# Performance work log

Hardware: AMD Instinct MI355X
Metric: run time of the kernel (lower is better)

## Reference

```python
import jax, jax.numpy as jnp
import numpy as np

N_EMBED = 1024
N_HEAD = 16
HEAD_SIZE = N_EMBED // N_HEAD  # 64
SEQ = 2048
BATCH = 2
EPS = 1e-5


def setup_inputs() -> dict:
    key = jax.random.key(0)
    ks = jax.random.split(key, 16)
    s = lambda fan_in: 1.0 / np.sqrt(fan_in)
    d, h, hs, f = N_EMBED, N_HEAD, HEAD_SIZE, 4 * N_EMBED
    return {
        "x": jax.random.normal(ks[0], (BATCH, SEQ, d), dtype=jnp.float32),
        # per-head QKV projections (no bias), stacked over heads: [H, D, hs]
        "wq": jax.random.normal(ks[1], (h, d, hs), dtype=jnp.float32) * s(d),
        "wk": jax.random.normal(ks[2], (h, d, hs), dtype=jnp.float32) * s(d),
        "wv": jax.random.normal(ks[3], (h, d, hs), dtype=jnp.float32) * s(d),
        "w_proj": jax.random.normal(ks[4], (d, d), dtype=jnp.float32) * s(d),
        "b_proj": jnp.zeros((d,), dtype=jnp.float32),
        "w1": jax.random.normal(ks[5], (d, f), dtype=jnp.float32) * s(d),
        "b1": jnp.zeros((f,), dtype=jnp.float32),
        "w2": jax.random.normal(ks[6], (f, d), dtype=jnp.float32) * s(f),
        "b2": jnp.zeros((d,), dtype=jnp.float32),
        "g1": jnp.ones((d,), dtype=jnp.float32),
        "be1": jnp.zeros((d,), dtype=jnp.float32),
        "g2": jnp.ones((d,), dtype=jnp.float32),
        "be2": jnp.zeros((d,), dtype=jnp.float32),
    }


def _layer_norm(x, gamma, beta):
    mu = jnp.mean(x, axis=-1, keepdims=True)
    var = jnp.mean(jnp.square(x - mu), axis=-1, keepdims=True)
    return (x - mu) * jax.lax.rsqrt(var + EPS) * gamma + beta


def reference(x, wq, wk, wv, w_proj, b_proj, w1, b1, w2, b2, g1, be1, g2, be2):
    B, S, D = x.shape
    # per-head projections (vectorized over heads): [B, H, S, hs]
    q = jnp.einsum("bsd,hdk->bhsk", x, wq)
    k = jnp.einsum("bsd,hdk->bhsk", x, wk)
    v = jnp.einsum("bsd,hdk->bhsk", x, wv)
    scale = HEAD_SIZE ** -0.5
    scores = jnp.einsum("bhsk,bhtk->bhst", q, k) * scale  # [B,H,S,S]
    causal = jnp.tril(jnp.ones((S, S), dtype=bool))
    scores = jnp.where(causal, scores, -jnp.inf)
    w = jax.nn.softmax(scores, axis=-1)  # dropout=0 -> identity
    attn = jnp.einsum("bhst,bhtk->bhsk", w, v)  # [B,H,S,hs]
    # concat heads (head-major ordering matches torch.cat over heads)
    attn = attn.transpose(0, 2, 1, 3).reshape(B, S, D)
    y = attn @ w_proj + b_proj
    x = _layer_norm(x + y, g1, be1)
    y = jax.nn.relu(x @ w1 + b1) @ w2 + b2
    x = _layer_norm(x + y, g2, be2)
    return x
```

## Files before the change

kernel.cpp:

```cpp
#include <hip/hip_runtime.h>


typedef unsigned short u16;
typedef unsigned int u32;
typedef __attribute__((ext_vector_type(8))) short bf16x8;
typedef __attribute__((ext_vector_type(4))) float f32x4;
typedef __attribute__((ext_vector_type(2))) u32 u32x2;
typedef __attribute__((ext_vector_type(4))) _Float16 f16x4;

#define MFMA16(a, b, c) __builtin_amdgcn_mfma_f32_16x16x32_bf16(a, b, c, 0, 0, 0)
#define MFMAH(a, b, c) __builtin_amdgcn_mfma_f32_16x16x16f16(a, b, c, 0, 0, 0)

__device__ __forceinline__ u16 f2b(float f) {
  unsigned int u = __builtin_bit_cast(unsigned int, f);
  u = (u + 0x7fffu + ((u >> 16) & 1u)) >> 16;
  return (u16)u;
}

__device__ __forceinline__ void gload_lds16(const u16* g, u16* l) {
  __builtin_amdgcn_global_load_lds((const __attribute__((address_space(1))) void*)g,
                                   (__attribute__((address_space(3))) void*)l, 16, 0, 0);
}

__device__ __forceinline__ u32 pkrtz(float lo, float hi) {
  return __builtin_bit_cast(u32, __builtin_amdgcn_cvt_pkrtz(lo, hi));
}

__device__ __forceinline__ f16x4 pack4h(float a, float b, float c, float d) {
  u32x2 r = {pkrtz(a, b), pkrtz(c, d)};
  return __builtin_bit_cast(f16x4, r);
}

__device__ __forceinline__ u16 f2h(float v) {
  return __builtin_bit_cast(u16, (_Float16)v);
}


__global__ __launch_bounds__(256) void castx_kernel(const float* __restrict__ src,
                                                    u16* __restrict__ dst) {
  int i = (blockIdx.x * 256 + threadIdx.x) * 4;
  float4 v = *(const float4*)(src + i);
  dst[i + 0] = f2b(v.x);
  dst[i + 1] = f2b(v.y);
  dst[i + 2] = f2b(v.z);
  dst[i + 3] = f2b(v.w);
}

__global__ __launch_bounds__(256) void tcast_kernel(const float* __restrict__ src,
                                                    u16* __restrict__ dst, int R, int C) {
  __shared__ float tile[32][33];
  int tx = threadIdx.x, ty = threadIdx.y;
  int r0 = blockIdx.y * 32, c0 = blockIdx.x * 32;
#pragma unroll
  for (int i = 0; i < 4; ++i)
    tile[ty + i * 8][tx] = src[(size_t)(r0 + ty + i * 8) * C + c0 + tx];
  __syncthreads();
#pragma unroll
  for (int i = 0; i < 4; ++i)
    dst[(size_t)(c0 + ty + i * 8) * R + r0 + tx] = f2b(tile[tx][ty + i * 8]);
}

__global__ __launch_bounds__(256) void tcast_qkv_kernel(const float* __restrict__ wq,
                                                        const float* __restrict__ wk,
                                                        const float* __restrict__ wv,
                                                        u16* __restrict__ dst) {
  __shared__ float tile[32][33];
  int tx = threadIdx.x, ty = threadIdx.y;
  int z = blockIdx.z;
  int p = z >> 4, h = z & 15;
  const float* src = (p == 0 ? wq : (p == 1 ? wk : wv)) + (size_t)h * 1024 * 64;
  float scale = (p == 0) ? 0.1803368801f : 1.0f;
  u16* dbase = dst + (size_t)(p * 1024 + h * 64) * 1024;
  int r0 = blockIdx.y * 32, c0 = blockIdx.x * 32;
#pragma unroll
  for (int i = 0; i < 4; ++i)
    tile[ty + i * 8][tx] = src[(size_t)(r0 + ty + i * 8) * 64 + c0 + tx];
  __syncthreads();
#pragma unroll
  for (int i = 0; i < 4; ++i)
    dbase[(size_t)(c0 + ty + i * 8) * 1024 + r0 + tx] = f2b(tile[tx][ty + i * 8] * scale);
}


template <int MODE>
__global__ __launch_bounds__(256) void gemm_bf16(const u16* __restrict__ A,
                                                 const u16* __restrict__ Bt, int M, int N,
                                                 int Kc, int lda,
                                                 const float* __restrict__ bias,
                                                 u16* __restrict__ outB, int ldc,
                                                 u16* __restrict__ vtg) {
  constexpr int BM = 128, BN = 128, BK = 64;
  constexpr int IM = 4, JN = 4;
  __shared__ u16 As[BM * BK];
  __shared__ u16 Bs[BN * BK];
  int t = threadIdx.x;
  int m0 = blockIdx.x * BM, n0 = blockIdx.y * BN;
  int kb = blockIdx.z * Kc;
  int lane = t & 63, wid = t >> 6;
  int wm = (wid >> 1) * 64, wn = (wid & 1) * 64;
  int m16 = lane & 15, quad = lane >> 4;
  int sw = m16 & 7;

  f32x4 acc[IM][JN] = {};

  for (int k0 = kb; k0 < kb + Kc; k0 += BK) {
    __syncthreads();
#pragma unroll
    for (int i = 0; i < 4; ++i) {
      int S = i * 256 + t;
      int row = S >> 3, c = S & 7;
      gload_lds16(&A[(size_t)(m0 + row) * lda + k0 + (c ^ (row & 7)) * 8],
                  &As[(i * 256 + wid * 64) * 8]);
    }
#pragma unroll
    for (int i = 0; i < 4; ++i) {
      int S = i * 256 + t;
      int row = S >> 3, c = S & 7;
      gload_lds16(&Bt[(size_t)(n0 + row) * lda + k0 + (c ^ (row & 7)) * 8],
                  &Bs[(i * 256 + wid * 64) * 8]);
    }
    __syncthreads();
#pragma unroll
    for (int kk = 0; kk < 2; ++kk) {
      bf16x8 af[IM], bfr[JN];
      int slot = (kk * 4 + quad) ^ sw;
#pragma unroll
      for (int i = 0; i < IM; ++i)
        af[i] = *(const bf16x8*)&As[(wm + i * 16 + m16) * BK + slot * 8];
#pragma unroll
      for (int j = 0; j < JN; ++j)
        bfr[j] = *(const bf16x8*)&Bs[(wn + j * 16 + m16) * BK + slot * 8];
#pragma unroll
      for (int i = 0; i < IM; ++i)
#pragma unroll
        for (int j = 0; j < JN; ++j) acc[i][j] = MFMA16(af[i], bfr[j], acc[i][j]);
    }
  }

  if (MODE == 3 && n0 >= 2048) {
#pragma unroll
    for (int i = 0; i < IM; ++i)
#pragma unroll
      for (int j = 0; j < JN; ++j) {
        int dg = n0 + wn + j * 16 + m16 - 2048;
        int hh = dg >> 6, dd = dg & 63;
        int token = m0 + wm + i * 16 + quad * 4;
        int bb = token >> 11, tt = token & 2047;
        u32x2 pv = {pkrtz(acc[i][j][0], acc[i][j][1]),
                    pkrtz(acc[i][j][2], acc[i][j][3])};
        *(u32x2*)&vtg[(((size_t)bb * 16 + hh) * 64 + dd) * 2048 + tt] = pv;
      }
    return;
  }

  u16* pb = (MODE == 4) ? outB + (size_t)blockIdx.z * M * N : outB;
#pragma unroll
  for (int i = 0; i < IM; ++i)
#pragma unroll
    for (int j = 0; j < JN; ++j) {
      int col = n0 + wn + j * 16 + m16;
      float bv = (MODE == 1) ? bias[col] : 0.0f;
#pragma unroll
      for (int r = 0; r < 4; ++r) {
        int row = m0 + wm + i * 16 + quad * 4 + r;
        float v = acc[i][j][r];
        if (MODE == 1) {
          v += bv;
          v = v > 0.0f ? v : 0.0f;
          pb[(size_t)row * ldc + col] = f2b(v);
        } else if (MODE == 4) {
          pb[(size_t)row * ldc + col] = f2h(v);
        } else {
          pb[(size_t)row * ldc + col] = f2b(v);
        }
      }
    }
}


__constant__ unsigned char R_QB[32] = {7, 6, 11, 11, 5, 10, 10, 9, 9, 4, 8,
                                       8, 3, 15, 15, 15, 15, 14, 14, 14, 13, 13,
                                       13, 13, 12, 12, 12, 2, 14, 12, 1, 0};
__constant__ unsigned char R_K0[32] = {0, 0, 0, 12, 0, 0, 11, 0, 10, 0, 0,
                                       9, 0, 0, 8, 16, 24, 0, 8, 16, 0, 7,
                                       14, 21, 0, 7, 14, 0, 24, 21, 0, 0};
__constant__ unsigned char R_NIT[32] = {16, 14, 12, 12, 12, 11, 11, 10, 10, 10, 9,
                                        9, 8, 8, 8, 8, 8, 8, 8, 8, 7, 7,
                                        7, 7, 7, 7, 7, 6, 6, 5, 4, 2};
__constant__ unsigned char R_ST[32] = {255, 255, 6, 7, 255, 4, 5, 2, 3, 255, 0,
                                       1, 255, 20, 21, 22, 23, 16, 17, 18, 12, 13,
                                       14, 15, 8, 9, 10, 255, 19, 11, 255, 255};
__constant__ unsigned char CB_BASE[8] = {0, 2, 4, 6, 8, 12, 16, 20};

__global__ __launch_bounds__(256) void attn_part(const u16* __restrict__ qk,
                                                 const u16* __restrict__ vtg,
                                                 u16* __restrict__ attn_out,
                                                 u16* __restrict__ opart,
                                                 float2* __restrict__ ml) {
  int rank = blockIdx.x >> 5, bh = blockIdx.x & 31;
  int qb = R_QB[rank];
  int k_start = R_K0[rank] * 64;
  int iters = R_NIT[rank];
  int st = R_ST[rank];
  int b = bh >> 4, h = bh & 15;

  int t = threadIdx.x, lane = t & 63, w = t >> 6;
  int m16 = lane & 15, quad = lane >> 4;
  int wq0 = qb * 128 + w * 32;

  __shared__ u16 Ks[2][64 * 64];
  __shared__ u16 Vs[2][64 * 64];

  bf16x8 qa[2][2];
#pragma unroll
  for (int qs = 0; qs < 2; ++qs) {
    const u16* qp = qk + (size_t)(b * 2048 + wq0 + qs * 16 + m16) * 2048 + h * 64;
    qa[qs][0] = *(const bf16x8*)&qp[quad * 8];
    qa[qs][1] = *(const bf16x8*)&qp[32 + quad * 8];
  }

  f32x4 oT[2][4] = {};
  f32x4 lacc[2] = {};
  float mrun[2] = {-1e30f, -1e30f};

  int row0 = t >> 3, c0 = t & 7;
  int row1 = 32 + row0;
  const u16* kbase = qk + (size_t)(b * 2048) * 2048 + 1024 + h * 64;
  const u16* vbase = vtg + ((size_t)(b * 16 + h) * 64) * 2048;
  int sw = m16 & 7;

#define STAGE_ASYNC(T0, BUF)                                                        \
  {                                                                                 \
    gload_lds16(&kbase[(size_t)((T0) + row0) * 2048 + (c0 ^ (row0 & 7)) * 8],       \
                &Ks[BUF][(w * 64) * 8]);                                            \
    gload_lds16(&kbase[(size_t)((T0) + row1) * 2048 + (c0 ^ (row1 & 7)) * 8],       \
                &Ks[BUF][(256 + w * 64) * 8]);                                      \
    gload_lds16(&vbase[(size_t)row0 * 2048 + (T0) + (c0 ^ (row0 & 7)) * 8],         \
                &Vs[BUF][(w * 64) * 8]);                                            \
    gload_lds16(&vbase[(size_t)row1 * 2048 + (T0) + (c0 ^ (row1 & 7)) * 8],         \
                &Vs[BUF][(256 + w * 64) * 8]);                                      \
  }

  STAGE_ASYNC(k_start, 0);
  __syncthreads();

  for (int it = 0; it < iters; ++it) {
    int t0 = k_start + it * 64;
    int cur = it & 1;
    if (it + 1 < iters) STAGE_ASYNC(t0 + 64, !cur);

    if (t0 <= wq0 + 31) {
      f32x4 sv[2][4];
#pragma unroll
      for (int ts = 0; ts < 4; ++ts) {
        bf16x8 ka0 = *(const bf16x8*)&Ks[cur][(ts * 16 + m16) * 64 + (quad ^ sw) * 8];
        bf16x8 ka1 =
            *(const bf16x8*)&Ks[cur][(ts * 16 + m16) * 64 + ((4 + quad) ^ sw) * 8];
#pragma unroll
        for (int qs = 0; qs < 2; ++qs) {
          f32x4 a = {};
          a = MFMA16(ka0, qa[qs][0], a);
          a = MFMA16(ka1, qa[qs][1], a);
          sv[qs][ts] = a;
        }
      }
      if (t0 + 63 > wq0) {
#pragma unroll
        for (int qs = 0; qs < 2; ++qs)
#pragma unroll
          for (int ts = 0; ts < 4; ++ts)
#pragma unroll
            for (int rr = 0; rr < 4; ++rr) {
              int key = t0 + ts * 16 + quad * 4 + rr;
              if (key > wq0 + qs * 16 + m16) sv[qs][ts][rr] = -3e38f;
            }
      }
#pragma unroll
      for (int qs = 0; qs < 2; ++qs) {
        float mx = fmaxf(fmaxf(sv[qs][0][0], sv[qs][0][1]),
                         fmaxf(sv[qs][0][2], sv[qs][0][3]));
#pragma unroll
        for (int ts = 1; ts < 4; ++ts)
          mx = fmaxf(mx, fmaxf(fmaxf(sv[qs][ts][0], sv[qs][ts][1]),
                               fmaxf(sv[qs][ts][2], sv[qs][ts][3])));
        mx = fmaxf(mx, __shfl_xor(mx, 16));
        mx = fmaxf(mx, __shfl_xor(mx, 32));
        float mnew = fmaxf(mrun[qs], mx);
        float alpha = exp2f(mrun[qs] - mnew);
        mrun[qs] = mnew;
        lacc[qs] *= alpha;
#pragma unroll
        for (int ds = 0; ds < 4; ++ds) oT[qs][ds] *= alpha;
      }
      f16x4 pf[2][4];
#pragma unroll
      for (int qs = 0; qs < 2; ++qs)
#pragma unroll
        for (int ts = 0; ts < 4; ++ts) {
          float p0 = exp2f(sv[qs][ts][0] - mrun[qs]);
          float p1 = exp2f(sv[qs][ts][1] - mrun[qs]);
          float p2 = exp2f(sv[qs][ts][2] - mrun[qs]);
          float p3 = exp2f(sv[qs][ts][3] - mrun[qs]);
          lacc[qs][0] += p0;
          lacc[qs][1] += p1;
          lacc[qs][2] += p2;
          lacc[qs][3] += p3;
          pf[qs][ts] = pack4h(p0, p1, p2, p3);
        }
#pragma unroll
      for (int ts = 0; ts < 4; ++ts)
#pragma unroll
        for (int ds = 0; ds < 4; ++ds) {
          f16x4 av = __builtin_bit_cast(
              f16x4, *(const u32x2*)&Vs[cur][(ds * 16 + m16) * 64 +
                                             (((ts * 2 + (quad >> 1)) ^ sw) * 8) +
                                             (quad & 1) * 4]);
          oT[0][ds] = MFMAH(av, pf[0][ts], oT[0][ds]);
          oT[1][ds] = MFMAH(av, pf[1][ts], oT[1][ds]);
        }
    }
    __syncthreads();
  }
#undef STAGE_ASYNC

  if (st == 255) {
#pragma unroll
    for (int qs = 0; qs < 2; ++qs) {
      float ls = lacc[qs][0] + lacc[qs][1] + lacc[qs][2] + lacc[qs][3];
      ls += __shfl_xor(ls, 16);
      ls += __shfl_xor(ls, 32);
      float rl = 1.0f / ls;
      int q = wq0 + qs * 16 + m16;
#pragma unroll
      for (int ds = 0; ds < 4; ++ds) {
        f32x4 o = oT[qs][ds];
        u32x2 ov = {(u32)f2b(o[0] * rl) | ((u32)f2b(o[1] * rl) << 16),
                    (u32)f2b(o[2] * rl) | ((u32)f2b(o[3] * rl) << 16)};
        *(u32x2*)&attn_out[(size_t)(b * 2048 + q) * 1024 + h * 64 + ds * 16 +
                           quad * 4] = ov;
      }
    }
  } else {
    size_t sbase = ((size_t)st * 32 + bh) * 128;
#pragma unroll
    for (int qs = 0; qs < 2; ++qs) {
      float ls = lacc[qs][0] + lacc[qs][1] + lacc[qs][2] + lacc[qs][3];
      ls += __shfl_xor(ls, 16);
      ls += __shfl_xor(ls, 32);
      int qloc = w * 32 + qs * 16 + m16;
#pragma unroll
      for (int ds = 0; ds < 4; ++ds) {
        f32x4 o = oT[qs][ds];
        u32x2 ov = {pkrtz(o[0], o[1]), pkrtz(o[2], o[3])};
        *(u32x2*)&opart[(sbase + qloc) * 64 + ds * 16 + quad * 4] = ov;
      }
      if (quad == 0) ml[sbase + qloc] = make_float2(mrun[qs], ls);
    }
  }
}

__global__ __launch_bounds__(256) void attn_comb(const u16* __restrict__ opart,
                                                 const float2* __restrict__ ml,
                                                 u16* __restrict__ attn_out) {
  int qb = 8 + blockIdx.x, bh = blockIdx.y;
  int b = bh >> 4, h = bh & 15;
  int nseg = (qb < 12) ? 2 : 4;
  int base = CB_BASE[qb - 8];
  int t = threadIdx.x;
  int q = t >> 1, dh = (t & 1) * 32;

  float m[4], l[4], wgt[4];
  float M = -3e38f;
  for (int s = 0; s < nseg; ++s) {
    float2 v = ml[((size_t)(base + s) * 32 + bh) * 128 + q];
    m[s] = v.x;
    l[s] = v.y;
    M = fmaxf(M, v.x);
  }
  float lsum = 0.0f;
  for (int s = 0; s < nseg; ++s) {
    wgt[s] = exp2f(m[s] - M);
    lsum += wgt[s] * l[s];
  }
  float rl = 1.0f / lsum;

  size_t orow = (size_t)(b * 2048 + qb * 128 + q) * 1024 + h * 64 + dh;
#pragma unroll 2
  for (int dd = 0; dd < 32; dd += 4) {
    float o0 = 0, o1 = 0, o2 = 0, o3 = 0;
    for (int s = 0; s < nseg; ++s) {
      f16x4 hv = __builtin_bit_cast(
          f16x4, *(const u32x2*)&opart[(((size_t)(base + s) * 32 + bh) * 128 + q) * 64 +
                                       dh + dd]);
      o0 += wgt[s] * (float)hv[0];
      o1 += wgt[s] * (float)hv[1];
      o2 += wgt[s] * (float)hv[2];
      o3 += wgt[s] * (float)hv[3];
    }
    u32x2 ov = {(u32)f2b(o0 * rl) | ((u32)f2b(o1 * rl) << 16),
                (u32)f2b(o2 * rl) | ((u32)f2b(o3 * rl) << 16)};
    *(u32x2*)&attn_out[orow + dd] = ov;
  }
}


__global__ __launch_bounds__(256) void ln_comb(const u16* __restrict__ parts, int np,
                                               const float* __restrict__ bias,
                                               const float* __restrict__ resid,
                                               const float* __restrict__ g,
                                               const float* __restrict__ be,
                                               float* __restrict__ outF,
                                               u16* __restrict__ outB) {
  int row = blockIdx.x;
  int t = threadIdx.x;
  size_t off = (size_t)row * 1024 + t * 4;
  float4 bv4 = *(const float4*)(bias + t * 4);
  float a0 = bv4.x, a1 = bv4.y, a2 = bv4.z, a3 = bv4.w;
  for (int c = 0; c < np; ++c) {
    f16x4 hv =
        __builtin_bit_cast(f16x4, *(const u32x2*)&parts[(size_t)c * 4096 * 1024 + off]);
    a0 += (float)hv[0];
    a1 += (float)hv[1];
    a2 += (float)hv[2];
    a3 += (float)hv[3];
  }
  float4 rv = *(const float4*)(resid + off);
  a0 += rv.x;
  a1 += rv.y;
  a2 += rv.z;
  a3 += rv.w;

  float s = a0 + a1 + a2 + a3;
  float sq = a0 * a0 + a1 * a1 + a2 * a2 + a3 * a3;
#pragma unroll
  for (int d = 1; d < 64; d <<= 1) {
    s += __shfl_xor(s, d);
    sq += __shfl_xor(sq, d);
  }
  __shared__ float red[8];
  int lane = t & 63, wid = t >> 6;
  if (lane == 0) {
    red[wid] = s;
    red[4 + wid] = sq;
  }
  __syncthreads();
  s = red[0] + red[1] + red[2] + red[3];
  sq = red[4] + red[5] + red[6] + red[7];
  float mu = s * (1.0f / 1024.0f);
  float var = sq * (1.0f / 1024.0f) - mu * mu;
  float rstd = rsqrtf(var + 1e-5f);
  float4 gv = *(const float4*)(g + t * 4);
  float4 bev = *(const float4*)(be + t * 4);
  float o0 = (a0 - mu) * rstd * gv.x + bev.x;
  float o1 = (a1 - mu) * rstd * gv.y + bev.y;
  float o2 = (a2 - mu) * rstd * gv.z + bev.z;
  float o3 = (a3 - mu) * rstd * gv.w + bev.w;
  if (outF) {
    float4 ov = {o0, o1, o2, o3};
    *(float4*)(outF + off) = ov;
  }
  if (outB) {
    outB[off + 0] = f2b(o0);
    outB[off + 1] = f2b(o1);
    outB[off + 2] = f2b(o2);
    outB[off + 3] = f2b(o3);
  }
}


extern "C" void kernel_launch(void* const* d_in, const int* in_sizes, int n_in,
                              void* d_out, int out_size, void* d_ws, size_t ws_size,
                              hipStream_t stream) {
  const float* x = (const float*)d_in[0];
  const float* wq = (const float*)d_in[1];
  const float* wk = (const float*)d_in[2];
  const float* wv = (const float*)d_in[3];
  const float* w_proj = (const float*)d_in[4];
  const float* b_proj = (const float*)d_in[5];
  const float* w1 = (const float*)d_in[6];
  const float* b1 = (const float*)d_in[7];
  const float* w2 = (const float*)d_in[8];
  const float* b2 = (const float*)d_in[9];
  const float* g1 = (const float*)d_in[10];
  const float* be1 = (const float*)d_in[11];
  const float* g2 = (const float*)d_in[12];
  const float* be2 = (const float*)d_in[13];
  float* out = (float*)d_out;

  const int M = 4096;
  char* w = (char*)d_ws;
  u16* Xbf = (u16*)w;        w += (size_t)M * 1024 * 2;
  u16* WqkvT = (u16*)w;      w += (size_t)3072 * 1024 * 2;
  u16* WprojT = (u16*)w;     w += (size_t)1024 * 1024 * 2;
  u16* W1T = (u16*)w;        w += (size_t)4096 * 1024 * 2;
  u16* X1b = (u16*)w;        w += (size_t)M * 1024 * 2;
  u16* W2T = (u16*)w;        w += (size_t)1024 * 4096 * 2;
  u16* QK = (u16*)w;         w += (size_t)M * 2048 * 2;
  u16* Vtg = (u16*)w;        w += (size_t)2 * 16 * 64 * 2048 * 2;
  u16* Attn = (u16*)w;       w += (size_t)M * 1024 * 2;
  float* X1f = (float*)w;    w += (size_t)M * 1024 * 4;

  u16* Pdown = Xbf;
  u16* Pproj = QK;
  u16* Hbuf = QK;
  u16* Opart = (u16*)X1f;
  float2* Ml = (float2*)((char*)X1f + (size_t)13 * 1024 * 1024);

  castx_kernel<<<M * 1024 / 1024, 256, 0, stream>>>(x, Xbf);
  tcast_qkv_kernel<<<dim3(2, 32, 48), dim3(32, 8), 0, stream>>>(wq, wk, wv, WqkvT);
  tcast_kernel<<<dim3(32, 32), dim3(32, 8), 0, stream>>>(w_proj, WprojT, 1024, 1024);
  tcast_kernel<<<dim3(128, 32), dim3(32, 8), 0, stream>>>(w1, W1T, 1024, 4096);
  tcast_kernel<<<dim3(32, 128), dim3(32, 8), 0, stream>>>(w2, W2T, 4096, 1024);

  gemm_bf16<3><<<dim3(32, 24, 1), 256, 0, stream>>>(Xbf, WqkvT, M, 3072, 1024, 1024,
                                                    nullptr, QK, 2048, Vtg);

  attn_part<<<1024, 256, 0, stream>>>(QK, Vtg, Attn, Opart, Ml);
  attn_comb<<<dim3(8, 32), 256, 0, stream>>>(Opart, Ml, Attn);

  gemm_bf16<4><<<dim3(32, 8, 2), 256, 0, stream>>>(Attn, WprojT, M, 1024, 512, 1024,
                                                   nullptr, Pproj, 1024, nullptr);
  ln_comb<<<M, 256, 0, stream>>>(Pproj, 2, b_proj, x, g1, be1, X1f, X1b);

  gemm_bf16<1><<<dim3(32, 32, 1), 256, 0, stream>>>(X1b, W1T, M, 4096, 1024, 1024, b1,
                                                    Hbuf, 4096, nullptr);

  gemm_bf16<4><<<dim3(32, 8, 4), 256, 0, stream>>>(Hbuf, W2T, M, 1024, 1024, 4096,
                                                   nullptr, Pdown, 1024, nullptr);
  ln_comb<<<M, 256, 0, stream>>>(Pdown, 4, b2, X1f, g2, be2, out, nullptr);
}
```

Before: 363.4 us.

## Load attention K/V straight to registers per wave, drop shared staging and barriers

The attention partial kernel no longer stages K and V tiles into shared memory with async global-to-LDS loads and block barriers. Each wave now loads its K fragments and V fragments directly from global memory into registers, with K double-buffered across iterations, and trims its iteration count to its own causal limit. Row sums are computed with an MFMA against a ones vector instead of scalar adds and shuffles. This removes the __syncthreads and LDS traffic and lets waves skip fully masked tiles on their own, at the cost of redundant global loads across the four waves, more register pressure, and less coalesced V reads.

```diff
diff --git a/kernel.cpp b/kernel.cpp
--- a/kernel.cpp
+++ b/kernel.cpp
@@ -200,7 +200,7 @@
   int rank = blockIdx.x >> 5, bh = blockIdx.x & 31;
   int qb = R_QB[rank];
   int k_start = R_K0[rank] * 64;
-  int iters = R_NIT[rank];
+  int nit_blk = R_NIT[rank];
   int st = R_ST[rank];
   int b = bh >> 4, h = bh & 15;
 
@@ -208,8 +208,8 @@
   int m16 = lane & 15, quad = lane >> 4;
   int wq0 = qb * 128 + w * 32;
 
-  __shared__ u16 Ks[2][64 * 64];
-  __shared__ u16 Vs[2][64 * 64];
+  int k_end = min(k_start + nit_blk * 64, wq0 + 32);
+  int iters = (k_end - k_start + 63) >> 6;
 
   bf16x8 qa[2][2];
 #pragma unroll
@@ -219,117 +219,113 @@
     qa[qs][1] = *(const bf16x8*)&qp[32 + quad * 8];
   }
 
+  const u16* kb = qk + ((size_t)(b * 2048 + m16) * 2048) + 1024 + h * 64 + quad * 8;
+  const u16* vb = vtg + ((size_t)(b * 16 + h) * 64 + m16) * 2048 + quad * 4;
+
   f32x4 oT[2][4] = {};
-  f32x4 lacc[2] = {};
+  f32x4 oL[2] = {};
   float mrun[2] = {-1e30f, -1e30f};
 
-  int row0 = t >> 3, c0 = t & 7;
-  int row1 = 32 + row0;
-  const u16* kbase = qk + (size_t)(b * 2048) * 2048 + 1024 + h * 64;
-  const u16* vbase = vtg + ((size_t)(b * 16 + h) * 64) * 2048;
-  int sw = m16 & 7;
-
-#define STAGE_ASYNC(T0, BUF)                                                        \
-  {                                                                                 \
-    gload_lds16(&kbase[(size_t)((T0) + row0) * 2048 + (c0 ^ (row0 & 7)) * 8],       \
-                &Ks[BUF][(w * 64) * 8]);                                            \
-    gload_lds16(&kbase[(size_t)((T0) + row1) * 2048 + (c0 ^ (row1 & 7)) * 8],       \
-                &Ks[BUF][(256 + w * 64) * 8]);                                      \
-    gload_lds16(&vbase[(size_t)row0 * 2048 + (T0) + (c0 ^ (row0 & 7)) * 8],         \
-                &Vs[BUF][(w * 64) * 8]);                                            \
-    gload_lds16(&vbase[(size_t)row1 * 2048 + (T0) + (c0 ^ (row1 & 7)) * 8],         \
-                &Vs[BUF][(256 + w * 64) * 8]);                                      \
-  }
-
-  STAGE_ASYNC(k_start, 0);
-  __syncthreads();
-
-  for (int it = 0; it < iters; ++it) {
-    int t0 = k_start + it * 64;
-    int cur = it & 1;
-    if (it + 1 < iters) STAGE_ASYNC(t0 + 64, !cur);
-
-    if (t0 <= wq0 + 31) {
-      f32x4 sv[2][4];
+  f16x4 ones;
+#pragma unroll
+  for (int j = 0; j < 4; ++j) ones[j] = (_Float16)1.0f;
+
+  bf16x8 kA[4][2], kB[4][2];
+  f16x4 vf[4][4];
+
+  auto loadK = [&](bf16x8(&KF)[4][2], int T0) {
+#pragma unroll
+    for (int ts = 0; ts < 4; ++ts) {
+      KF[ts][0] = *(const bf16x8*)&kb[(size_t)(T0 + ts * 16) * 2048];
+      KF[ts][1] = *(const bf16x8*)&kb[(size_t)(T0 + ts * 16) * 2048 + 32];
+    }
+  };
+  auto loadV = [&](int T0) {
+#pragma unroll
+    for (int ds = 0; ds < 4; ++ds)
+#pragma unroll
+      for (int ts = 0; ts < 4; ++ts)
+        vf[ds][ts] = *(const f16x4*)&vb[(size_t)ds * 32768 + T0 + ts * 16];
+  };
+  auto body = [&](const bf16x8(&KF)[4][2], int T0) {
+    f32x4 sv[2][4];
+#pragma unroll
+    for (int ts = 0; ts < 4; ++ts)
+#pragma unroll
+      for (int qs = 0; qs < 2; ++qs) {
+        f32x4 a = {};
+        a = MFMA16(KF[ts][0], qa[qs][0], a);
+        a = MFMA16(KF[ts][1], qa[qs][1], a);
+        sv[qs][ts] = a;
+      }
+    if (T0 + 63 > wq0) {
+#pragma unroll
+      for (int qs = 0; qs < 2; ++qs)
+#pragma unroll
+        for (int ts = 0; ts < 4; ++ts)
+#pragma unroll
+          for (int rr = 0; rr < 4; ++rr) {
+            int key = T0 + ts * 16 + quad * 4 + rr;
+            if (key > wq0 + qs * 16 + m16) sv[qs][ts][rr] = -3e38f;
+          }
+    }
+    f16x4 pf[2][4];
+#pragma unroll
+    for (int qs = 0; qs < 2; ++qs) {
+      float mx = fmaxf(fmaxf(sv[qs][0][0], sv[qs][0][1]),
+                       fmaxf(sv[qs][0][2], sv[qs][0][3]));
+#pragma unroll
+      for (int ts = 1; ts < 4; ++ts)
+        mx = fmaxf(mx, fmaxf(fmaxf(sv[qs][ts][0], sv[qs][ts][1]),
+                             fmaxf(sv[qs][ts][2], sv[qs][ts][3])));
+      mx = fmaxf(mx, __shfl_xor(mx, 16));
+      mx = fmaxf(mx, __shfl_xor(mx, 32));
+      float mnew = fmaxf(mrun[qs], mx);
+      float alpha = exp2f(mrun[qs] - mnew);
+      mrun[qs] = mnew;
+      oL[qs] *= alpha;
+#pragma unroll
+      for (int ds = 0; ds < 4; ++ds) oT[qs][ds] *= alpha;
 #pragma unroll
       for (int ts = 0; ts < 4; ++ts) {
-        bf16x8 ka0 = *(const bf16x8*)&Ks[cur][(ts * 16 + m16) * 64 + (quad ^ sw) * 8];
-        bf16x8 ka1 =
-            *(const bf16x8*)&Ks[cur][(ts * 16 + m16) * 64 + ((4 + quad) ^ sw) * 8];
-#pragma unroll
-        for (int qs = 0; qs < 2; ++qs) {
-          f32x4 a = {};
-          a = MFMA16(ka0, qa[qs][0], a);
-          a = MFMA16(ka1, qa[qs][1], a);
-          sv[qs][ts] = a;
-        }
-      }
-      if (t0 + 63 > wq0) {
-#pragma unroll
-        for (int qs = 0; qs < 2; ++qs)
-#pragma unroll
-          for (int ts = 0; ts < 4; ++ts)
-#pragma unroll
-            for (int rr = 0; rr < 4; ++rr) {
-              int key = t0 + ts * 16 + quad * 4 + rr;
-              if (key > wq0 + qs * 16 + m16) sv[qs][ts][rr] = -3e38f;
-            }
-      }
-#pragma unroll
-      for (int qs = 0; qs < 2; ++qs) {
-        float mx = fmaxf(fmaxf(sv[qs][0][0], sv[qs][0][1]),
-                         fmaxf(sv[qs][0][2], sv[qs][0][3]));
-#pragma unroll
-        for (int ts = 1; ts < 4; ++ts)
-          mx = fmaxf(mx, fmaxf(fmaxf(sv[qs][ts][0], sv[qs][ts][1]),
-                               fmaxf(sv[qs][ts][2], sv[qs][ts][3])));
-        mx = fmaxf(mx, __shfl_xor(mx, 16));
-        mx = fmaxf(mx, __shfl_xor(mx, 32));
-        float mnew = fmaxf(mrun[qs], mx);
-        float alpha = exp2f(mrun[qs] - mnew);
-        mrun[qs] = mnew;
-        lacc[qs] *= alpha;
-#pragma unroll
-        for (int ds = 0; ds < 4; ++ds) oT[qs][ds] *= alpha;
-      }
-      f16x4 pf[2][4];
-#pragma unroll
-      for (int qs = 0; qs < 2; ++qs)
-#pragma unroll
-        for (int ts = 0; ts < 4; ++ts) {
-          float p0 = exp2f(sv[qs][ts][0] - mrun[qs]);
-          float p1 = exp2f(sv[qs][ts][1] - mrun[qs]);
-          float p2 = exp2f(sv[qs][ts][2] - mrun[qs]);
-          float p3 = exp2f(sv[qs][ts][3] - mrun[qs]);
-          lacc[qs][0] += p0;
-          lacc[qs][1] += p1;
-          lacc[qs][2] += p2;
-          lacc[qs][3] += p3;
-          pf[qs][ts] = pack4h(p0, p1, p2, p3);
-        }
-#pragma unroll
-      for (int ts = 0; ts < 4; ++ts)
-#pragma unroll
-        for (int ds = 0; ds < 4; ++ds) {
-          f16x4 av = __builtin_bit_cast(
-              f16x4, *(const u32x2*)&Vs[cur][(ds * 16 + m16) * 64 +
-                                             (((ts * 2 + (quad >> 1)) ^ sw) * 8) +
-                                             (quad & 1) * 4]);
-          oT[0][ds] = MFMAH(av, pf[0][ts], oT[0][ds]);
-          oT[1][ds] = MFMAH(av, pf[1][ts], oT[1][ds]);
-        }
-    }
-    __syncthreads();
-  }
-#undef STAGE_ASYNC
+        float p0 = exp2f(sv[qs][ts][0] - mnew);
+        float p1 = exp2f(sv[qs][ts][1] - mnew);
+        float p2 = exp2f(sv[qs][ts][2] - mnew);
+        float p3 = exp2f(sv[qs][ts][3] - mnew);
+        pf[qs][ts] = pack4h(p0, p1, p2, p3);
+        oL[qs] = MFMAH(ones, pf[qs][ts], oL[qs]);
+      }
+    }
+#pragma unroll
+    for (int ts = 0; ts < 4; ++ts)
+#pragma unroll
+      for (int ds = 0; ds < 4; ++ds) {
+        oT[0][ds] = MFMAH(vf[ds][ts], pf[0][ts], oT[0][ds]);
+        oT[1][ds] = MFMAH(vf[ds][ts], pf[1][ts], oT[1][ds]);
+      }
+  };
+
+  loadK(kA, k_start);
+  int it = 0, t0 = k_start;
+  while (true) {
+    if (it + 1 < iters) loadK(kB, t0 + 64);
+    loadV(t0);
+    body(kA, t0);
+    ++it;
+    t0 += 64;
+    if (it >= iters) break;
+    if (it + 1 < iters) loadK(kA, t0 + 64);
+    loadV(t0);
+    body(kB, t0);
+    ++it;
+    t0 += 64;
+    if (it >= iters) break;
+  }
 
   if (st == 255) {
 #pragma unroll
     for (int qs = 0; qs < 2; ++qs) {
-      float ls = lacc[qs][0] + lacc[qs][1] + lacc[qs][2] + lacc[qs][3];
-      ls += __shfl_xor(ls, 16);
-      ls += __shfl_xor(ls, 32);
-      float rl = 1.0f / ls;
+      float rl = 1.0f / oL[qs][0];
       int q = wq0 + qs * 16 + m16;
 #pragma unroll
       for (int ds = 0; ds < 4; ++ds) {
@@ -344,9 +340,6 @@
     size_t sbase = ((size_t)st * 32 + bh) * 128;
 #pragma unroll
     for (int qs = 0; qs < 2; ++qs) {
-      float ls = lacc[qs][0] + lacc[qs][1] + lacc[qs][2] + lacc[qs][3];
-      ls += __shfl_xor(ls, 16);
-      ls += __shfl_xor(ls, 32);
       int qloc = w * 32 + qs * 16 + m16;
 #pragma unroll
       for (int ds = 0; ds < 4; ++ds) {
@@ -354,7 +347,7 @@
         u32x2 ov = {pkrtz(o[0], o[1]), pkrtz(o[2], o[3])};
         *(u32x2*)&opart[(sbase + qloc) * 64 + ds * 16 + quad * 4] = ov;
       }
-      if (quad == 0) ml[sbase + qloc] = make_float2(mrun[qs], ls);
+      if (quad == 0) ml[sbase + qloc] = make_float2(mrun[qs], oL[qs][0]);
     }
   }
 }
```

Result: slower. 408.4 us (+12.4%).
